# Optimization experiments

Measured on AMD Instinct MI355X. Metric: run time of the kernel, lower is better.

## Reference

```python
import jax, jax.numpy as jnp
import numpy as np

D_MODEL = 256   # dim // 2
DIM = 512
D_INNER = 512   # expand=2 * d_model
D_STATE = 16
D_CONV = 4
DT_RANK = 16    # ceil(d_model/16)
N_LAYERS = 2
H_RES, W_RES = 16, 16
EPS = 1e-5


def silu(v):
    return v * jax.nn.sigmoid(v)


def setup_inputs() -> dict:
    key = jax.random.key(0)
    ks = jax.random.split(key, 12)
    Bsz, T, N = 2, 4, 256
    x = jax.random.normal(ks[0], (Bsz, 1 + T * N, DIM), jnp.float32)
    skip = jax.random.normal(ks[1], (Bsz, 1 + 4 * T * N, D_MODEL), jnp.float32)
    sc = lambda k, shape, s: jax.random.normal(k, shape, jnp.float32) * s
    exp_w = sc(ks[2], (2 * DIM, DIM), 0.02)            # PatchExpanding2D.expansion (no bias)
    ln_g = jnp.ones((DIM // 2,), jnp.float32)
    ln_b = jnp.zeros((DIM // 2,), jnp.float32)
    cls_w = sc(ks[3], (DIM // 2, DIM), 0.02)
    cls_b = jnp.zeros((DIM // 2,), jnp.float32)
    in_proj_w = sc(ks[4], (N_LAYERS, 2 * D_INNER, D_MODEL), 0.02)
    conv_w = sc(ks[5], (N_LAYERS, D_INNER, D_CONV), 0.1)  # depthwise causal conv
    conv_b = jnp.zeros((N_LAYERS, D_INNER), jnp.float32)
    xproj_w = sc(ks[6], (N_LAYERS, DT_RANK + 2 * D_STATE, D_INNER), 0.02)
    dt_w = sc(ks[7], (N_LAYERS, D_INNER, DT_RANK), 0.1)
    dt_b = sc(ks[8], (N_LAYERS, D_INNER), 0.1)
    A_log = jnp.log(jnp.broadcast_to(jnp.arange(1, D_STATE + 1, dtype=jnp.float32), (N_LAYERS, D_INNER, D_STATE)))
    Dp = jnp.ones((N_LAYERS, D_INNER), jnp.float32)
    out_w = sc(ks[9], (N_LAYERS, D_MODEL, D_INNER), 0.02)
    bn_g = jnp.ones((D_MODEL,), jnp.float32)
    bn_b = jnp.zeros((D_MODEL,), jnp.float32)
    return {"x": x, "skip_connection": skip, "exp_w": exp_w, "ln_g": ln_g, "ln_b": ln_b,
            "cls_w": cls_w, "cls_b": cls_b, "in_proj_w": in_proj_w, "conv_w": conv_w,
            "conv_b": conv_b, "xproj_w": xproj_w, "dt_w": dt_w, "dt_b": dt_b,
            "A_log": A_log, "Dp": Dp, "out_w": out_w, "bn_g": bn_g, "bn_b": bn_b,
            "B": 2, "T": 4, "N": 256}


def mamba_layer(u, Wi, cw, cb, Wx, Wdt, bdt, A_log, Dd, Wo):
    # u: [B, L, d_model]
    Bb, L, _ = u.shape
    xz = jnp.einsum('bld,ed->ble', u, Wi)            # [B, L, 2*d_inner]
    xi, z = jnp.split(xz, 2, axis=-1)
    # depthwise causal conv1d (pad left d_conv-1)
    xp = jnp.pad(xi, ((0, 0), (D_CONV - 1, 0), (0, 0)))
    xc = cb + sum(cw[:, k] * xp[:, k:k + L, :] for k in range(D_CONV))
    xi = silu(xc)
    dbc = jnp.einsum('bld,ed->ble', xi, Wx)          # [B, L, dt_rank + 2*d_state]
    dt = dbc[..., :DT_RANK]
    Bm = dbc[..., DT_RANK:DT_RANK + D_STATE]
    Cm = dbc[..., DT_RANK + D_STATE:]
    delta = jax.nn.softplus(jnp.einsum('blr,dr->bld', dt, Wdt) + bdt)  # [B, L, d_inner]
    A = -jnp.exp(A_log)                              # [d_inner, d_state]

    def step(h, inp):
        d_t, B_t, C_t, x_t = inp                     # [B,d], [B,n], [B,n], [B,d]
        h = h * jnp.exp(d_t[..., None] * A) + d_t[..., None] * B_t[:, None, :] * x_t[..., None]
        y = jnp.einsum('bdn,bn->bd', h, C_t)
        return h, y

    h0 = jnp.zeros((Bb, D_INNER, D_STATE), u.dtype)
    xs = (jnp.swapaxes(delta, 0, 1), jnp.swapaxes(Bm, 0, 1),
          jnp.swapaxes(Cm, 0, 1), jnp.swapaxes(xi, 0, 1))
    _, ys = jax.lax.scan(step, h0, xs)               # ys: [L, B, d_inner]
    y = jnp.swapaxes(ys, 0, 1) + xi * Dd
    y = y * silu(z)
    return jnp.einsum('bld,od->blo', y, Wo)          # [B, L, d_model]


def reference(x, skip_connection, exp_w, ln_g, ln_b, cls_w, cls_b, in_proj_w, conv_w,
              conv_b, xproj_w, dt_w, dt_b, A_log, Dp, out_w, bn_g, bn_b, B, T, N):
    cls = x[:B, :1, :]                               # [B, 1, dim]
    toks = x[:, 1:, :].reshape(x.shape[0], T, N, DIM)
    # patch expanding: Linear dim -> 2*dim, then 2x2 pixel shuffle, LayerNorm(dim//2)
    e = jnp.einsum('btnm,em->btne', toks, exp_w)     # [B, T, N, 2*dim]
    m = (2 * DIM) // 4                               # dim // 2
    e = e.reshape(-1, T, H_RES, W_RES, 2, 2, m)
    e = jnp.transpose(e, (0, 1, 2, 4, 3, 5, 6)).reshape(-1, T, 4 * N, m)
    mu = e.mean(-1, keepdims=True)
    var = e.var(-1, keepdims=True)
    e = (e - mu) / jnp.sqrt(var + EPS) * ln_g + ln_b
    e = e.reshape(e.shape[0], T * 4 * N, m)
    cls = jnp.einsum('bom,em->boe', cls, cls_w) + cls_b
    xx = jnp.concatenate([cls, e], axis=1) + skip_connection
    for i in range(N_LAYERS):
        xx = mamba_layer(xx, in_proj_w[i], conv_w[i], conv_b[i], xproj_w[i],
                         dt_w[i], dt_b[i], A_log[i], Dp[i], out_w[i])
    # BatchNorm1d over channels (training-mode batch stats, biased variance)
    mu = xx.mean(axis=(0, 1))
    var = xx.var(axis=(0, 1))
    xx = (xx - mu) / jnp.sqrt(var + EPS) * bn_g + bn_b
    return xx, 4 * N
```

## Files before the change

### kernel.cpp

```cpp
#include <hip/hip_runtime.h>
#include <hip/hip_bf16.h>
#include <math.h>

#define L_TOT 4097
#define BSZ 2
#define ROWS (BSZ*L_TOT)
#define NSEG 128
#define SEGLEN 33

typedef __bf16 bf16x8 __attribute__((ext_vector_type(8)));
typedef float  f32x4  __attribute__((ext_vector_type(4)));
#define ASTR 56
#define AST2 72

__device__ __forceinline__ float sigmoidf_(float v){ return 1.0f/(1.0f+__expf(-v)); }
__device__ __forceinline__ float siluf_(float v){ return v * sigmoidf_(v); }
__device__ __forceinline__ unsigned short bfbits(float f){
    __bf16 h = (__bf16)f;
    return __builtin_bit_cast(unsigned short, h);
}

__global__ __launch_bounds__(256) void cvt4(
    const float* __restrict__ w0, const float* __restrict__ w1,
    const float* __restrict__ w2, const float* __restrict__ w3,
    __bf16* __restrict__ o0, __bf16* __restrict__ o1,
    __bf16* __restrict__ o2, __bf16* __restrict__ o3)
{
    long i = ((long)blockIdx.x*256 + threadIdx.x)*8;
    const float* src; __bf16* dst; long off;
    if (i < 524288)        { src = w0; dst = o0; off = i; }
    else if (i < 1048576)  { src = w1; dst = o1; off = i - 524288; }
    else if (i < 1310720)  { src = w2; dst = o2; off = i - 1048576; }
    else if (i < 1359872)  { src = w3; dst = o3; off = i - 1310720; }
    else return;
    float4 a = *(const float4*)(src+off), b = *(const float4*)(src+off+4);
    bf16x8 o;
    o[0]=(__bf16)a.x; o[1]=(__bf16)a.y; o[2]=(__bf16)a.z; o[3]=(__bf16)a.w;
    o[4]=(__bf16)b.x; o[5]=(__bf16)b.y; o[6]=(__bf16)b.z; o[7]=(__bf16)b.w;
    *(bf16x8*)(dst+off) = o;
}

__global__ __launch_bounds__(256) void cvt_gather_x(
    const float* __restrict__ x, __bf16* __restrict__ out)
{
    long i = ((long)blockIdx.x*256 + threadIdx.x)*8;
    if (i >= 2048L*512) return;
    int row = (int)(i >> 9), col = (int)(i & 511);
    long srow = row + (row >> 10) + 1;
    const float* src = x + srow*512 + col;
    float4 a = *(const float4*)src, b = *(const float4*)(src+4);
    bf16x8 o;
    o[0]=(__bf16)a.x; o[1]=(__bf16)a.y; o[2]=(__bf16)a.z; o[3]=(__bf16)a.w;
    o[4]=(__bf16)b.x; o[5]=(__bf16)b.y; o[6]=(__bf16)b.z; o[7]=(__bf16)b.w;
    *(bf16x8*)(out+i) = o;
}

template<int SMODE>
__global__ __launch_bounds__(256) void gemm_bf16(
    const __bf16* __restrict__ A, const __bf16* __restrict__ W,
    float* __restrict__ C, __bf16* __restrict__ C2, int M, int N, int K)
{
    __shared__ __bf16 Als[128*ASTR];
    __shared__ __bf16 Wls[64*ASTR];
    const int tid = threadIdx.x;
    const int lane = tid & 63, w = tid >> 6;
    const int n0 = blockIdx.x*64, m0 = blockIdx.y*128;

    f32x4 acc[2][4] = {};
    const int arow = tid >> 1, ahalf = tid & 1;
    const int wrow = tid >> 2, wseg = tid & 3;
    const int fr = lane & 15, fc = lane >> 4;

    for (int k0 = 0; k0 < K; k0 += 32) {
        bf16x8 av0 = {}, av1 = {};
        if (m0 + arow < M) {
            const __bf16* src = A + (long)(m0+arow)*K + k0 + ahalf*16;
            av0 = *(const bf16x8*)src;
            av1 = *(const bf16x8*)(src+8);
        }
        bf16x8 wv = *(const bf16x8*)(W + (long)(n0+wrow)*K + k0 + wseg*8);
        __syncthreads();
        *(bf16x8*)&Als[arow*ASTR + ahalf*16]     = av0;
        *(bf16x8*)&Als[arow*ASTR + ahalf*16 + 8] = av1;
        *(bf16x8*)&Wls[wrow*ASTR + wseg*8]       = wv;
        __syncthreads();

        bf16x8 a0 = *(const bf16x8*)&Als[(w*32 +      fr)*ASTR + fc*8];
        bf16x8 a1 = *(const bf16x8*)&Als[(w*32 + 16 + fr)*ASTR + fc*8];
        #pragma unroll
        for (int j = 0; j < 4; j++) {
            bf16x8 bv = *(const bf16x8*)&Wls[(j*16 + fr)*ASTR + fc*8];
            acc[0][j] = __builtin_amdgcn_mfma_f32_16x16x32_bf16(a0, bv, acc[0][j], 0,0,0);
            acc[1][j] = __builtin_amdgcn_mfma_f32_16x16x32_bf16(a1, bv, acc[1][j], 0,0,0);
        }
    }
    #pragma unroll
    for (int i = 0; i < 2; i++) {
        #pragma unroll
        for (int rr = 0; rr < 4; rr++) {
            int grow = m0 + w*32 + i*16 + fc*4 + rr;
            if (grow < M) {
                #pragma unroll
                for (int j = 0; j < 4; j++) {
                    float v = acc[i][j][rr];
                    long o = (long)grow*N + n0 + j*16 + fr;
                    if (SMODE != 2) C[o] = v;
                    if (SMODE != 0) C2[o] = (__bf16)v;
                }
            }
        }
    }
}

__global__ __launch_bounds__(256) void gemm_bf16_128(
    const __bf16* __restrict__ A, const __bf16* __restrict__ W,
    __bf16* __restrict__ C2, int M, int N, int K)
{
    __shared__ __bf16 Als[128*AST2];
    __shared__ __bf16 Wls[128*AST2];
    const int tid = threadIdx.x;
    const int lane = tid & 63, w = tid >> 6;
    const int n0 = blockIdx.x*128, m0 = blockIdx.y*128;
    const int fr = lane & 15, fc = lane >> 4;
    const int row2 = tid >> 1, half = tid & 1;

    f32x4 acc[2][8] = {};

    for (int k0 = 0; k0 < K; k0 += 64) {
        bf16x8 av[4], wv[4];
        const bool aok = (m0 + row2) < M;
        const __bf16* asrc = A + (long)(m0+row2)*K + k0 + half*32;
        const __bf16* wsrc = W + (long)(n0+row2)*K + k0 + half*32;
        #pragma unroll
        for (int e = 0; e < 4; e++) {
            av[e] = aok ? *(const bf16x8*)(asrc + e*8) : (bf16x8){};
            wv[e] = *(const bf16x8*)(wsrc + e*8);
        }
        __syncthreads();
        #pragma unroll
        for (int e = 0; e < 4; e++) {
            *(bf16x8*)&Als[row2*AST2 + half*32 + e*8] = av[e];
            *(bf16x8*)&Wls[row2*AST2 + half*32 + e*8] = wv[e];
        }
        __syncthreads();
        #pragma unroll
        for (int s = 0; s < 2; s++) {
            bf16x8 a0 = *(const bf16x8*)&Als[(w*32 +      fr)*AST2 + s*32 + fc*8];
            bf16x8 a1 = *(const bf16x8*)&Als[(w*32 + 16 + fr)*AST2 + s*32 + fc*8];
            #pragma unroll
            for (int j = 0; j < 8; j++) {
                bf16x8 bv = *(const bf16x8*)&Wls[(j*16 + fr)*AST2 + s*32 + fc*8];
                acc[0][j] = __builtin_amdgcn_mfma_f32_16x16x32_bf16(a0, bv, acc[0][j], 0,0,0);
                acc[1][j] = __builtin_amdgcn_mfma_f32_16x16x32_bf16(a1, bv, acc[1][j], 0,0,0);
            }
        }
    }
    #pragma unroll
    for (int i = 0; i < 2; i++) {
        #pragma unroll
        for (int rr = 0; rr < 4; rr++) {
            int grow = m0 + w*32 + i*16 + fc*4 + rr;
            if (grow < M) {
                #pragma unroll
                for (int j = 0; j < 8; j++)
                    C2[(long)grow*N + n0 + j*16 + fr] = (__bf16)acc[i][j][rr];
            }
        }
    }
}

__global__ __launch_bounds__(128) void gemm_dbc(
    const __bf16* __restrict__ A, const __bf16* __restrict__ W,
    float* __restrict__ C, int M)
{
    __shared__ __bf16 Als[64*ASTR];
    __shared__ __bf16 Wls[48*ASTR];
    const int tid = threadIdx.x;
    const int lane = tid & 63, w = tid >> 6;
    const int m0 = blockIdx.x*64;
    f32x4 acc[2][3] = {};

    const int arow = tid >> 1, ahalf = tid & 1;
    const int fr = lane & 15, fc = lane >> 4;

    for (int k0 = 0; k0 < 512; k0 += 32) {
        bf16x8 av0 = {}, av1 = {};
        if (m0 + arow < M) {
            const __bf16* src = A + (long)(m0+arow)*512 + k0 + ahalf*16;
            av0 = *(const bf16x8*)src;
            av1 = *(const bf16x8*)(src+8);
        }
        bf16x8 wv0 = {}, wv1 = {};
        if (tid < 96) {
            const __bf16* src = W + (long)(tid>>1)*512 + k0 + (tid&1)*16;
            wv0 = *(const bf16x8*)src;
            wv1 = *(const bf16x8*)(src+8);
        }
        __syncthreads();
        *(bf16x8*)&Als[arow*ASTR + ahalf*16]     = av0;
        *(bf16x8*)&Als[arow*ASTR + ahalf*16 + 8] = av1;
        if (tid < 96) {
            *(bf16x8*)&Wls[(tid>>1)*ASTR + (tid&1)*16]     = wv0;
            *(bf16x8*)&Wls[(tid>>1)*ASTR + (tid&1)*16 + 8] = wv1;
        }
        __syncthreads();

        bf16x8 a0 = *(const bf16x8*)&Als[(w*32 +      fr)*ASTR + fc*8];
        bf16x8 a1 = *(const bf16x8*)&Als[(w*32 + 16 + fr)*ASTR + fc*8];
        #pragma unroll
        for (int j = 0; j < 3; j++) {
            bf16x8 bv = *(const bf16x8*)&Wls[(j*16 + fr)*ASTR + fc*8];
            acc[0][j] = __builtin_amdgcn_mfma_f32_16x16x32_bf16(a0, bv, acc[0][j], 0,0,0);
            acc[1][j] = __builtin_amdgcn_mfma_f32_16x16x32_bf16(a1, bv, acc[1][j], 0,0,0);
        }
    }
    #pragma unroll
    for (int i = 0; i < 2; i++) {
        #pragma unroll
        for (int rr = 0; rr < 4; rr++) {
            int grow = m0 + w*32 + i*16 + fc*4 + rr;
            if (grow < M) {
                #pragma unroll
                for (int j = 0; j < 3; j++)
                    C[(long)grow*48 + j*16 + fr] = acc[i][j][rr];
            }
        }
    }
}

__global__ __launch_bounds__(256) void delta_k(
    const float* __restrict__ dbc, const float* __restrict__ Wdt,
    const float* __restrict__ bdt, const __bf16* __restrict__ xib,
    unsigned* __restrict__ pdx)
{
    const int d0 = threadIdx.x, d1 = threadIdx.x + 256;
    const int r0 = blockIdx.x*8;
    f32x4 wa[4], wb[4];
    #pragma unroll
    for (int q = 0; q < 4; q++) {
        wa[q] = *(const f32x4*)(Wdt + d0*16 + q*4);
        wb[q] = *(const f32x4*)(Wdt + d1*16 + q*4);
    }
    const float b0 = bdt[d0], b1 = bdt[d1];
    #pragma unroll
    for (int rr = 0; rr < 8; rr++) {
        int row = r0 + rr;
        if (row >= ROWS) return;
        const f32x4* p = (const f32x4*)(dbc + (long)row*48);
        f32x4 t0 = p[0], t1 = p[1], t2 = p[2], t3 = p[3];
        float s0 = b0, s1 = b1;
        #pragma unroll
        for (int e = 0; e < 4; e++) {
            s0 += wa[0][e]*t0[e] + wa[1][e]*t1[e] + wa[2][e]*t2[e] + wa[3][e]*t3[e];
            s1 += wb[0][e]*t0[e] + wb[1][e]*t1[e] + wb[2][e]*t2[e] + wb[3][e]*t3[e];
        }
        float dl0 = (s0 > 20.f) ? s0 : log1pf(__expf(s0));
        float dl1 = (s1 > 20.f) ? s1 : log1pf(__expf(s1));
        unsigned x0 = __builtin_bit_cast(unsigned short, xib[(long)row*512 + d0]);
        unsigned x1 = __builtin_bit_cast(unsigned short, xib[(long)row*512 + d1]);
        pdx[(long)row*512 + d0] = (unsigned)bfbits(dl0) | (x0 << 16);
        pdx[(long)row*512 + d1] = (unsigned)bfbits(dl1) | (x1 << 16);
    }
}

__global__ __launch_bounds__(256) void rearrange_ln_cls(
    const __bf16* __restrict__ e_buf, const float* __restrict__ x,
    const float* __restrict__ cls_w, const float* __restrict__ cls_b,
    const float* __restrict__ ln_g, const float* __restrict__ ln_b,
    const float* __restrict__ skip, float* __restrict__ xx,
    __bf16* __restrict__ xxb)
{
    const int blk = blockIdx.x;
    const int b = blk / L_TOT;
    const int q = blk % L_TOT;
    const int c = threadIdx.x;

    if (q == 0) {
        __shared__ float xr[512];
        const float* xrow = x + (long)b*1025*512;
        xr[c] = xrow[c]; xr[c+256] = xrow[c+256];
        __syncthreads();
        float acc = cls_b[c];
        const float4* wrow = (const float4*)(cls_w + (long)c*512);
        #pragma unroll 8
        for (int m4 = 0; m4 < 128; m4++) {
            float4 wv = wrow[m4];
            float4 xv = *(const float4*)&xr[m4*4];
            acc += wv.x*xv.x + wv.y*xv.y + wv.z*xv.z + wv.w*xv.w;
        }
        long o = (long)b*L_TOT*256 + c;
        float v = acc + skip[o];
        xx[o] = v; xxb[o] = (__bf16)v;
        return;
    }
    const int t  = (q-1) >> 10;
    const int p  = (q-1) & 1023;
    const int h  = p >> 6;
    const int a  = (p >> 5) & 1;
    const int w  = (p >> 1) & 15;
    const int bb = p & 1;
    const long tok = (long)b*1024 + t*256 + h*16 + w;
    float v = (float)e_buf[tok*1024 + a*512 + bb*256 + c];

    float s = v, s2 = v*v;
    #pragma unroll
    for (int o = 32; o > 0; o >>= 1) { s += __shfl_xor(s, o); s2 += __shfl_xor(s2, o); }
    __shared__ float ps[4], ps2[4];
    __shared__ float mu_s, rs_s;
    const int wv = threadIdx.x >> 6;
    if ((threadIdx.x & 63) == 0) { ps[wv] = s; ps2[wv] = s2; }
    __syncthreads();
    if (threadIdx.x == 0) {
        float S = ps[0]+ps[1]+ps[2]+ps[3];
        float S2 = ps2[0]+ps2[1]+ps2[2]+ps2[3];
        float mu = S * (1.f/256.f);
        float var = S2 * (1.f/256.f) - mu*mu;
        mu_s = mu; rs_s = rsqrtf(var + 1e-5f);
    }
    __syncthreads();
    long o = ((long)b*L_TOT + q)*256 + c;
    float outv = (v - mu_s)*rs_s*ln_g[c] + ln_b[c] + skip[o];
    xx[o] = outv; xxb[o] = (__bf16)outv;
}

__global__ __launch_bounds__(256) void conv_silu_split(
    const __bf16* __restrict__ xzb, const float* __restrict__ cw,
    const float* __restrict__ cb, __bf16* __restrict__ xib,
    __bf16* __restrict__ zsb)
{
    const int tid = threadIdx.x;
    const int c = tid & 127;
    const long r0 = ((long)blockIdx.x*2 + (tid >> 7))*8;
    if (r0 >= ROWS) return;

    if (c < 64) {
        const int d0 = c*8;
        float wreg[4][8], breg[8];
        #pragma unroll
        for (int e = 0; e < 8; e++) {
            breg[e] = cb[d0+e];
            #pragma unroll
            for (int k = 0; k < 4; k++) wreg[k][e] = cw[(d0+e)*4 + k];
        }
        bf16x8 win[4];
        #pragma unroll
        for (int j = 0; j < 3; j++) {
            long rr = r0 - 3 + j;
            win[j] = (rr >= 0) ? *(const bf16x8*)&xzb[rr*1024 + d0] : (bf16x8){};
        }
        #pragma unroll
        for (int rr = 0; rr < 8; rr++) {
            long rl = r0 + rr;
            if (rl >= ROWS) break;
            win[3] = *(const bf16x8*)&xzb[rl*1024 + d0];
            int l = (int)(rl % L_TOT);
            float acc[8];
            #pragma unroll
            for (int e = 0; e < 8; e++) acc[e] = breg[e];
            #pragma unroll
            for (int k = 0; k < 4; k++) {
                if (l + k - 3 >= 0) {
                    #pragma unroll
                    for (int e = 0; e < 8; e++)
                        acc[e] += wreg[k][e]*(float)win[k][e];
                }
            }
            bf16x8 o;
            #pragma unroll
            for (int e = 0; e < 8; e++) o[e] = (__bf16)siluf_(acc[e]);
            *(bf16x8*)&xib[rl*512 + d0] = o;
            win[0] = win[1]; win[1] = win[2]; win[2] = win[3];
        }
    } else {
        const int d0 = (c - 64)*8;
        #pragma unroll
        for (int rr = 0; rr < 8; rr++) {
            long rl = r0 + rr;
            if (rl >= ROWS) break;
            bf16x8 v = *(const bf16x8*)&xzb[rl*1024 + 512 + d0];
            bf16x8 o;
            #pragma unroll
            for (int e = 0; e < 8; e++) o[e] = (__bf16)siluf_((float)v[e]);
            *(bf16x8*)&zsb[rl*512 + d0] = o;
        }
    }
}

__global__ __launch_bounds__(256) void scan_p1(
    const unsigned* __restrict__ pdx,
    const float* __restrict__ dbc, const float* __restrict__ A_log,
    float* __restrict__ segH, float* __restrict__ segP)
{
    __shared__ unsigned pdxS[SEGLEN*64];
    __shared__ float bS[SEGLEN*16];
    const int blk = blockIdx.x;
    const int seg = blk >> 4;
    const int b   = (blk >> 3) & 1;
    const int dbase = (blk & 7)*64;
    const int tid = threadIdx.x;
    const int l0 = seg*SEGLEN;
    const int nl = min(l0 + SEGLEN, L_TOT) - l0;
    const int nlc = nl > 0 ? nl : 0;

    for (int cc = tid; cc < nlc*16; cc += 256) {
        int l = cc >> 4, qq = cc & 15;
        *(uint4*)&pdxS[l*64 + qq*4] =
            *(const uint4*)&pdx[((long)b*L_TOT + l0 + l)*512 + dbase + qq*4];
    }
    for (int cc = tid; cc < nlc*4; cc += 256) {
        int l = cc >> 2, qq = cc & 3;
        *(f32x4*)&bS[l*16 + qq*4] =
            *(const f32x4*)&dbc[((long)b*L_TOT + l0 + l)*48 + 16 + qq*4];
    }
    __syncthreads();

    const int dl_ = tid >> 2;
    const int d = dbase + dl_;
    const int ng = tid & 3;
    f32x4 Al = *(const f32x4*)(A_log + d*16 + ng*4);
    float Ar[4] = {-__expf(Al[0]), -__expf(Al[1]), -__expf(Al[2]), -__expf(Al[3])};
    float h[4] = {0,0,0,0};
    float P[4] = {1,1,1,1};
    for (int l = 0; l < nlc; l++) {
        unsigned v = pdxS[l*64 + dl_];
        float dl = __uint_as_float(v << 16);
        float xv = __uint_as_float(v & 0xffff0000u);
        f32x4 Bv = *(const f32x4*)&bS[l*16 + ng*4];
        float dx = dl*xv;
        #pragma unroll
        for (int n = 0; n < 4; n++) {
            float E = __expf(dl*Ar[n]);
            h[n] = h[n]*E + dx*Bv[n];
            P[n] *= E;
        }
    }
    long off = ((long)(seg*2 + b)*512 + d)*16 + ng*4;
    *(f32x4*)&segH[off] = f32x4{h[0],h[1],h[2],h[3]};
    *(f32x4*)&segP[off] = f32x4{P[0],P[1],P[2],P[3]};
}

__global__ __launch_bounds__(256) void scan_p2(
    float* __restrict__ segH, const float* __restrict__ segP)
{
    const int idx = blockIdx.x*256 + threadIdx.x;
    float carry = 0.f;
    for (int s0 = 0; s0 < NSEG; s0 += 8) {
        float hh[8], pp[8];
        #pragma unroll
        for (int j = 0; j < 8; j++) {
            long o = (long)(s0+j)*16384 + idx;
            hh[j] = segH[o]; pp[j] = segP[o];
        }
        #pragma unroll
        for (int j = 0; j < 8; j++) {
            long o = (long)(s0+j)*16384 + idx;
            segH[o] = carry;
            carry = pp[j]*carry + hh[j];
        }
    }
}

__global__ __launch_bounds__(256) void scan_p3(
    const unsigned* __restrict__ pdx,
    const float* __restrict__ dbc, const float* __restrict__ A_log,
    const float* __restrict__ segH, const float* __restrict__ Dp,
    const __bf16* __restrict__ zsb, __bf16* __restrict__ yb)
{
    __shared__ unsigned pdxS[SEGLEN*64];
    __shared__ float bcS[SEGLEN*32];
    __shared__ __bf16 zS[SEGLEN*64];
    __shared__ __bf16 yS[SEGLEN*64];
    const int blk = blockIdx.x;
    const int seg = blk >> 4;
    const int b   = (blk >> 3) & 1;
    const int dbase = (blk & 7)*64;
    const int tid = threadIdx.x;
    const int l0 = seg*SEGLEN;
    const int nl = min(l0 + SEGLEN, L_TOT) - l0;
    const int nlc = nl > 0 ? nl : 0;
    if (nlc == 0) return;

    for (int cc = tid; cc < nlc*16; cc += 256) {
        int l = cc >> 4, qq = cc & 15;
        *(uint4*)&pdxS[l*64 + qq*4] =
            *(const uint4*)&pdx[((long)b*L_TOT + l0 + l)*512 + dbase + qq*4];
    }
    for (int cc = tid; cc < nlc*8; cc += 256) {
        int l = cc >> 3, qq = cc & 7;
        *(f32x4*)&bcS[l*32 + qq*4] =
            *(const f32x4*)&dbc[((long)b*L_TOT + l0 + l)*48 + 16 + qq*4];
    }
    for (int cc = tid; cc < nlc*8; cc += 256) {
        int l = cc >> 3, qq = cc & 7;
        *(bf16x8*)&zS[l*64 + qq*8] =
            *(const bf16x8*)&zsb[((long)b*L_TOT + l0 + l)*512 + dbase + qq*8];
    }
    __syncthreads();

    const int dl_ = tid >> 2;
    const int d = dbase + dl_;
    const int ng = tid & 3;
    f32x4 Al = *(const f32x4*)(A_log + d*16 + ng*4);
    float Ar[4] = {-__expf(Al[0]), -__expf(Al[1]), -__expf(Al[2]), -__expf(Al[3])};
    long off = ((long)(seg*2 + b)*512 + d)*16 + ng*4;
    f32x4 h4 = *(const f32x4*)&segH[off];
    float h[4] = {h4[0], h4[1], h4[2], h4[3]};
    const float Dd = Dp[d];
    for (int l = 0; l < nlc; l++) {
        unsigned v = pdxS[l*64 + dl_];
        float dl = __uint_as_float(v << 16);
        float xv = __uint_as_float(v & 0xffff0000u);
        f32x4 Bv = *(const f32x4*)&bcS[l*32 + ng*4];
        f32x4 Cv = *(const f32x4*)&bcS[l*32 + 16 + ng*4];
        float dx = dl*xv;
        float y = 0.f;
        #pragma unroll
        for (int n = 0; n < 4; n++) {
            float E = __expf(dl*Ar[n]);
            h[n] = h[n]*E + dx*Bv[n];
            y += h[n]*Cv[n];
        }
        y += __shfl_xor(y, 1);
        y += __shfl_xor(y, 2);
        if (ng == 0) {
            float z = (float)zS[l*64 + dl_];
            yS[l*64 + dl_] = (__bf16)((y + xv*Dd)*z);
        }
    }
    __syncthreads();
    for (int cc = tid; cc < nlc*8; cc += 256) {
        int l = cc >> 3, qq = cc & 7;
        *(bf16x8*)&yb[((long)b*L_TOT + l0 + l)*512 + dbase + qq*8] =
            *(bf16x8*)&yS[l*64 + qq*8];
    }
}

__global__ void zero_stats(float* __restrict__ stats) { stats[threadIdx.x] = 0.f; }

__global__ __launch_bounds__(256) void bn_reduce(
    const float* __restrict__ xx, float* __restrict__ stats)
{
    const int c = threadIdx.x;
    float s = 0.f, s2 = 0.f;
    for (int r = blockIdx.x; r < ROWS; r += gridDim.x) {
        float v = xx[(long)r*256 + c];
        s += v; s2 += v*v;
    }
    atomicAdd(&stats[c], s);
    atomicAdd(&stats[256 + c], s2);
}

__global__ __launch_bounds__(256) void bn_apply(
    const float* __restrict__ xx, const float* __restrict__ stats,
    const float* __restrict__ g, const float* __restrict__ bta,
    float* __restrict__ out)
{
    long idx = (long)blockIdx.x*256 + threadIdx.x;
    if (idx == 0) out[(long)ROWS*256] = 1024.0f;
    if (idx >= (long)ROWS*256) return;
    int c = (int)(idx & 255);
    float mu = stats[c] * (1.f/ROWS);
    float var = stats[256 + c] * (1.f/ROWS) - mu*mu;
    out[idx] = (xx[idx] - mu)*rsqrtf(var + 1e-5f)*g[c] + bta[c];
}

extern "C" void kernel_launch(void* const* d_in, const int* in_sizes, int n_in,
                              void* d_out, int out_size, void* d_ws, size_t ws_size,
                              hipStream_t stream)
{
    const float* x        = (const float*)d_in[0];
    const float* skip     = (const float*)d_in[1];
    const float* exp_w    = (const float*)d_in[2];
    const float* ln_g     = (const float*)d_in[3];
    const float* ln_b     = (const float*)d_in[4];
    const float* cls_w    = (const float*)d_in[5];
    const float* cls_b    = (const float*)d_in[6];
    const float* in_proj_w= (const float*)d_in[7];
    const float* conv_w   = (const float*)d_in[8];
    const float* conv_b   = (const float*)d_in[9];
    const float* xproj_w  = (const float*)d_in[10];
    const float* dt_w     = (const float*)d_in[11];
    const float* dt_b     = (const float*)d_in[12];
    const float* A_log    = (const float*)d_in[13];
    const float* Dp       = (const float*)d_in[14];
    const float* out_w    = (const float*)d_in[15];
    const float* bn_g     = (const float*)d_in[16];
    const float* bn_b     = (const float*)d_in[17];

    float* ws = (float*)d_ws;
    float* xx    = ws;
    float* dbc   = xx + 2097664;
    float* segH  = dbc + 393312;
    float* segP  = segH + 2097152;
    float* stats = segP + 2097152;
    unsigned* pdx = (unsigned*)(stats + 512);
    __bf16* expWb = (__bf16*)(pdx + 4195328);
    __bf16* inWb  = expWb + 524288;
    __bf16* outWb = inWb + 524288;
    __bf16* xpWb  = outWb + 262144;
    __bf16* xxb   = xpWb + 49152;
    __bf16* xzb   = xxb + 2097664;
    __bf16* e_b   = xzb;
    __bf16* xib   = xzb + 8390656;
    __bf16* Axb   = xib;
    __bf16* zsb   = xib + 4195328;
    __bf16* yb    = zsb + 4195328;
    float* out    = (float*)d_out;

    cvt4<<<(1359872/8 + 255)/256, 256, 0, stream>>>(
        exp_w, in_proj_w, out_w, xproj_w, expWb, inWb, outWb, xpWb);
    cvt_gather_x<<<(1048576/8)/256, 256, 0, stream>>>(x, Axb);

    gemm_bf16<2><<<dim3(16, 16), 256, 0, stream>>>(
        Axb, expWb, nullptr, e_b, 2048, 1024, 512);
    rearrange_ln_cls<<<ROWS, 256, 0, stream>>>(
        e_b, x, cls_w, cls_b, ln_g, ln_b, skip, xx, xxb);

    for (int layer = 0; layer < 2; layer++) {
        gemm_bf16_128<<<dim3(8, 65), 256, 0, stream>>>(
            xxb, inWb + layer*262144, xzb, ROWS, 1024, 256);
        conv_silu_split<<<513, 256, 0, stream>>>(
            xzb, conv_w + layer*512*4, conv_b + layer*512, xib, zsb);
        gemm_dbc<<<(ROWS + 63)/64, 128, 0, stream>>>(
            xib, xpWb + layer*24576, dbc, ROWS);
        delta_k<<<(ROWS + 7)/8, 256, 0, stream>>>(
            dbc, dt_w + layer*512*16, dt_b + layer*512, xib, pdx);
        scan_p1<<<NSEG*16, 256, 0, stream>>>(
            pdx, dbc, A_log + layer*512*16, segH, segP);
        scan_p2<<<64, 256, 0, stream>>>(segH, segP);
        scan_p3<<<NSEG*16, 256, 0, stream>>>(
            pdx, dbc, A_log + layer*512*16, segH, Dp + layer*512, zsb, yb);
        if (layer == 0) {
            gemm_bf16<1><<<dim3(4, 65), 256, 0, stream>>>(
                yb, outWb, xx, xxb, ROWS, 256, 512);
        } else {
            gemm_bf16<0><<<dim3(4, 65), 256, 0, stream>>>(
                yb, outWb + 131072, xx, nullptr, ROWS, 256, 512);
        }
    }

    zero_stats<<<1, 512, 0, stream>>>(stats);
    bn_reduce<<<128, 256, 0, stream>>>(xx, stats);
    bn_apply<<<((long)ROWS*256 + 255)/256 + 1, 256, 0, stream>>>(xx, stats, bn_g, bn_b, out);
}
```

Before: 406.9 us.

## Fuse silu into in_proj epilogue, merge xproj with delta, drop fp32 residual

The in_proj GEMM now writes the x half and silu(z) half into separate bf16 buffers, so the conv kernel only handles the x half. The x-projection GEMM and the delta/softplus computation are fused into one kernel that stages a full 64-row tile in shared memory and emits B/C plus the packed delta/x words. The fp32 residual copy xx is dropped in favour of bf16 only, and LayerNorm/cls uses one wavefront per row with vector loads. These changes cut launches and global traffic, at the cost of lower precision in the final BatchNorm input and a large shared-memory footprint in the fused xproj kernel.

Result: slower. 498.8 us (+22.6%).

```diff
diff --git a/kernel.cpp b/kernel.cpp
--- a/kernel.cpp
+++ b/kernel.cpp
@@ -12,6 +12,7 @@
 typedef float  f32x4  __attribute__((ext_vector_type(4)));
 #define ASTR 56
 #define AST2 72
+#define XSTR 520
 
 __device__ __forceinline__ float sigmoidf_(float v){ return 1.0f/(1.0f+__expf(-v)); }
 __device__ __forceinline__ float siluf_(float v){ return v * sigmoidf_(v); }
@@ -55,10 +56,9 @@
     *(bf16x8*)(out+i) = o;
 }
 
-template<int SMODE>
 __global__ __launch_bounds__(256) void gemm_bf16(
     const __bf16* __restrict__ A, const __bf16* __restrict__ W,
-    float* __restrict__ C, __bf16* __restrict__ C2, int M, int N, int K)
+    __bf16* __restrict__ C2, int M, int N, int K)
 {
     __shared__ __bf16 Als[128*ASTR];
     __shared__ __bf16 Wls[64*ASTR];
@@ -101,20 +101,16 @@
             int grow = m0 + w*32 + i*16 + fc*4 + rr;
             if (grow < M) {
                 #pragma unroll
-                for (int j = 0; j < 4; j++) {
-                    float v = acc[i][j][rr];
-                    long o = (long)grow*N + n0 + j*16 + fr;
-                    if (SMODE != 2) C[o] = v;
-                    if (SMODE != 0) C2[o] = (__bf16)v;
-                }
+                for (int j = 0; j < 4; j++)
+                    C2[(long)grow*N + n0 + j*16 + fr] = (__bf16)acc[i][j][rr];
             }
         }
     }
 }
 
-__global__ __launch_bounds__(256) void gemm_bf16_128(
+__global__ __launch_bounds__(256) void gemm_inproj(
     const __bf16* __restrict__ A, const __bf16* __restrict__ W,
-    __bf16* __restrict__ C2, int M, int N, int K)
+    __bf16* __restrict__ xhb, __bf16* __restrict__ zsb, int M, int K)
 {
     __shared__ __bf16 Als[128*AST2];
     __shared__ __bf16 Wls[128*AST2];
@@ -155,111 +151,94 @@
             }
         }
     }
+    const bool xhalf = (n0 < 512);
+    const int cbase = xhalf ? n0 : (n0 - 512);
     #pragma unroll
     for (int i = 0; i < 2; i++) {
         #pragma unroll
         for (int rr = 0; rr < 4; rr++) {
             int grow = m0 + w*32 + i*16 + fc*4 + rr;
             if (grow < M) {
-                #pragma unroll
-                for (int j = 0; j < 8; j++)
-                    C2[(long)grow*N + n0 + j*16 + fr] = (__bf16)acc[i][j][rr];
+                if (xhalf) {
+                    #pragma unroll
+                    for (int j = 0; j < 8; j++)
+                        xhb[(long)grow*512 + cbase + j*16 + fr] = (__bf16)acc[i][j][rr];
+                } else {
+                    #pragma unroll
+                    for (int j = 0; j < 8; j++)
+                        zsb[(long)grow*512 + cbase + j*16 + fr] = (__bf16)siluf_(acc[i][j][rr]);
+                }
             }
         }
     }
 }
 
-__global__ __launch_bounds__(128) void gemm_dbc(
-    const __bf16* __restrict__ A, const __bf16* __restrict__ W,
-    float* __restrict__ C, int M)
-{
-    __shared__ __bf16 Als[64*ASTR];
-    __shared__ __bf16 Wls[48*ASTR];
+__global__ __launch_bounds__(256) void xproj_fused(
+    const __bf16* __restrict__ xib, const __bf16* __restrict__ Wx,
+    const float* __restrict__ Wdt, const float* __restrict__ bdt,
+    float* __restrict__ BC, unsigned* __restrict__ pdx)
+{
+    __shared__ __bf16 At[64*XSTR];
+    __shared__ __bf16 Wls[48*XSTR];
+    __shared__ float dtS[64*16];
     const int tid = threadIdx.x;
     const int lane = tid & 63, w = tid >> 6;
-    const int m0 = blockIdx.x*64;
-    f32x4 acc[2][3] = {};
-
-    const int arow = tid >> 1, ahalf = tid & 1;
+    const long r0 = (long)blockIdx.x*64;
     const int fr = lane & 15, fc = lane >> 4;
 
+    for (int idx = tid; idx < 64*64; idx += 256) {
+        int r = idx >> 6, c8 = idx & 63;
+        bf16x8 v = (r0 + r < ROWS) ? *(const bf16x8*)&xib[(r0+r)*512 + c8*8]
+                                   : (bf16x8){};
+        *(bf16x8*)&At[r*XSTR + c8*8] = v;
+    }
+    for (int idx = tid; idx < 48*64; idx += 256) {
+        int r = idx >> 6, c8 = idx & 63;
+        *(bf16x8*)&Wls[r*XSTR + c8*8] = *(const bf16x8*)&Wx[r*512 + c8*8];
+    }
+    __syncthreads();
+
+    f32x4 acc[3] = {};
     for (int k0 = 0; k0 < 512; k0 += 32) {
-        bf16x8 av0 = {}, av1 = {};
-        if (m0 + arow < M) {
-            const __bf16* src = A + (long)(m0+arow)*512 + k0 + ahalf*16;
-            av0 = *(const bf16x8*)src;
-            av1 = *(const bf16x8*)(src+8);
-        }
-        bf16x8 wv0 = {}, wv1 = {};
-        if (tid < 96) {
-            const __bf16* src = W + (long)(tid>>1)*512 + k0 + (tid&1)*16;
-            wv0 = *(const bf16x8*)src;
-            wv1 = *(const bf16x8*)(src+8);
-        }
-        __syncthreads();
-        *(bf16x8*)&Als[arow*ASTR + ahalf*16]     = av0;
-        *(bf16x8*)&Als[arow*ASTR + ahalf*16 + 8] = av1;
-        if (tid < 96) {
-            *(bf16x8*)&Wls[(tid>>1)*ASTR + (tid&1)*16]     = wv0;
-            *(bf16x8*)&Wls[(tid>>1)*ASTR + (tid&1)*16 + 8] = wv1;
-        }
-        __syncthreads();
-
-        bf16x8 a0 = *(const bf16x8*)&Als[(w*32 +      fr)*ASTR + fc*8];
-        bf16x8 a1 = *(const bf16x8*)&Als[(w*32 + 16 + fr)*ASTR + fc*8];
+        bf16x8 a = *(const bf16x8*)&At[(w*16 + fr)*XSTR + k0 + fc*8];
         #pragma unroll
         for (int j = 0; j < 3; j++) {
-            bf16x8 bv = *(const bf16x8*)&Wls[(j*16 + fr)*ASTR + fc*8];
-            acc[0][j] = __builtin_amdgcn_mfma_f32_16x16x32_bf16(a0, bv, acc[0][j], 0,0,0);
-            acc[1][j] = __builtin_amdgcn_mfma_f32_16x16x32_bf16(a1, bv, acc[1][j], 0,0,0);
-        }
-    }
-    #pragma unroll
-    for (int i = 0; i < 2; i++) {
-        #pragma unroll
-        for (int rr = 0; rr < 4; rr++) {
-            int grow = m0 + w*32 + i*16 + fc*4 + rr;
-            if (grow < M) {
-                #pragma unroll
-                for (int j = 0; j < 3; j++)
-                    C[(long)grow*48 + j*16 + fr] = acc[i][j][rr];
-            }
-        }
-    }
-}
-
-__global__ __launch_bounds__(256) void delta_k(
-    const float* __restrict__ dbc, const float* __restrict__ Wdt,
-    const float* __restrict__ bdt, const __bf16* __restrict__ xib,
-    unsigned* __restrict__ pdx)
-{
-    const int d0 = threadIdx.x, d1 = threadIdx.x + 256;
-    const int r0 = blockIdx.x*8;
-    f32x4 wa[4], wb[4];
-    #pragma unroll
-    for (int q = 0; q < 4; q++) {
-        wa[q] = *(const f32x4*)(Wdt + d0*16 + q*4);
-        wb[q] = *(const f32x4*)(Wdt + d1*16 + q*4);
-    }
-    const float b0 = bdt[d0], b1 = bdt[d1];
-    #pragma unroll
-    for (int rr = 0; rr < 8; rr++) {
-        int row = r0 + rr;
-        if (row >= ROWS) return;
-        const f32x4* p = (const f32x4*)(dbc + (long)row*48);
-        f32x4 t0 = p[0], t1 = p[1], t2 = p[2], t3 = p[3];
-        float s0 = b0, s1 = b1;
-        #pragma unroll
-        for (int e = 0; e < 4; e++) {
-            s0 += wa[0][e]*t0[e] + wa[1][e]*t1[e] + wa[2][e]*t2[e] + wa[3][e]*t3[e];
-            s1 += wb[0][e]*t0[e] + wb[1][e]*t1[e] + wb[2][e]*t2[e] + wb[3][e]*t3[e];
-        }
-        float dl0 = (s0 > 20.f) ? s0 : log1pf(__expf(s0));
-        float dl1 = (s1 > 20.f) ? s1 : log1pf(__expf(s1));
-        unsigned x0 = __builtin_bit_cast(unsigned short, xib[(long)row*512 + d0]);
-        unsigned x1 = __builtin_bit_cast(unsigned short, xib[(long)row*512 + d1]);
-        pdx[(long)row*512 + d0] = (unsigned)bfbits(dl0) | (x0 << 16);
-        pdx[(long)row*512 + d1] = (unsigned)bfbits(dl1) | (x1 << 16);
+            bf16x8 bv = *(const bf16x8*)&Wls[(j*16 + fr)*XSTR + k0 + fc*8];
+            acc[j] = __builtin_amdgcn_mfma_f32_16x16x32_bf16(a, bv, acc[j], 0,0,0);
+        }
+    }
+    #pragma unroll
+    for (int rr = 0; rr < 4; rr++) {
+        int lrow = w*16 + fc*4 + rr;
+        long grow = r0 + lrow;
+        dtS[lrow*16 + fr] = acc[0][rr];
+        if (grow < ROWS) {
+            BC[grow*32 + fr]      = acc[1][rr];
+            BC[grow*32 + 16 + fr] = acc[2][rr];
+        }
+    }
+    __syncthreads();
+
+    #pragma unroll
+    for (int rep = 0; rep < 2; rep++) {
+        const int d = tid + rep*256;
+        f32x4 wa0 = *(const f32x4*)(Wdt + d*16);
+        f32x4 wa1 = *(const f32x4*)(Wdt + d*16 + 4);
+        f32x4 wa2 = *(const f32x4*)(Wdt + d*16 + 8);
+        f32x4 wa3 = *(const f32x4*)(Wdt + d*16 + 12);
+        const float bia = bdt[d];
+        for (int r = 0; r < 64; r++) {
+            long grow = r0 + r;
+            if (grow >= ROWS) break;
+            const float* dt = &dtS[r*16];
+            float s = bia;
+            #pragma unroll
+            for (int e = 0; e < 4; e++)
+                s += wa0[e]*dt[e] + wa1[e]*dt[4+e] + wa2[e]*dt[8+e] + wa3[e]*dt[12+e];
+            float dl = (s > 20.f) ? s : log1pf(__expf(s));
+            unsigned xb = __builtin_bit_cast(unsigned short, At[r*XSTR + d]);
+            pdx[grow*512 + d] = (unsigned)bfbits(dl) | (xb << 16);
+        }
     }
 }
 
@@ -267,128 +246,119 @@
     const __bf16* __restrict__ e_buf, const float* __restrict__ x,
     const float* __restrict__ cls_w, const float* __restrict__ cls_b,
     const float* __restrict__ ln_g, const float* __restrict__ ln_b,
-    const float* __restrict__ skip, float* __restrict__ xx,
-    __bf16* __restrict__ xxb)
-{
-    const int blk = blockIdx.x;
-    const int b = blk / L_TOT;
-    const int q = blk % L_TOT;
-    const int c = threadIdx.x;
+    const float* __restrict__ skip, __bf16* __restrict__ xxb)
+{
+    const int wv = threadIdx.x >> 6, lane = threadIdx.x & 63;
+    const int qg = blockIdx.x*4 + wv;
+    if (qg >= ROWS) return;
+    const int b = qg / L_TOT, q = qg % L_TOT;
+    const long obase = (long)qg*256;
 
     if (q == 0) {
-        __shared__ float xr[512];
-        const float* xrow = x + (long)b*1025*512;
-        xr[c] = xrow[c]; xr[c+256] = xrow[c+256];
-        __syncthreads();
-        float acc = cls_b[c];
-        const float4* wrow = (const float4*)(cls_w + (long)c*512);
-        #pragma unroll 8
-        for (int m4 = 0; m4 < 128; m4++) {
-            float4 wv = wrow[m4];
-            float4 xv = *(const float4*)&xr[m4*4];
-            acc += wv.x*xv.x + wv.y*xv.y + wv.z*xv.z + wv.w*xv.w;
-        }
-        long o = (long)b*L_TOT*256 + c;
-        float v = acc + skip[o];
-        xx[o] = v; xxb[o] = (__bf16)v;
+        const float* xr = x + (long)b*1025*512;
+        #pragma unroll
+        for (int i = 0; i < 4; i++) {
+            int c = lane + i*64;
+            float acc = cls_b[c];
+            const float4* wr = (const float4*)(cls_w + (long)c*512);
+            #pragma unroll 8
+            for (int m4 = 0; m4 < 128; m4++) {
+                float4 wv4 = wr[m4];
+                float4 xv4 = *(const float4*)&xr[m4*4];
+                acc += wv4.x*xv4.x + wv4.y*xv4.y + wv4.z*xv4.z + wv4.w*xv4.w;
+            }
+            xxb[obase + c] = (__bf16)(acc + skip[obase + c]);
+        }
         return;
     }
     const int t  = (q-1) >> 10;
     const int p  = (q-1) & 1023;
     const int h  = p >> 6;
     const int a  = (p >> 5) & 1;
-    const int w  = (p >> 1) & 15;
+    const int w_ = (p >> 1) & 15;
     const int bb = p & 1;
-    const long tok = (long)b*1024 + t*256 + h*16 + w;
-    float v = (float)e_buf[tok*1024 + a*512 + bb*256 + c];
-
-    float s = v, s2 = v*v;
+    const long tok = (long)b*1024 + t*256 + h*16 + w_;
+    const __bf16* src = e_buf + tok*1024 + a*512 + bb*256 + lane*4;
+    float v[4];
+    {
+        ushort2 u0 = *(const ushort2*)src;
+        ushort2 u1 = *(const ushort2*)(src+2);
+        v[0] = (float)__builtin_bit_cast(__bf16, u0.x);
+        v[1] = (float)__builtin_bit_cast(__bf16, u0.y);
+        v[2] = (float)__builtin_bit_cast(__bf16, u1.x);
+        v[3] = (float)__builtin_bit_cast(__bf16, u1.y);
+    }
+    float s = v[0]+v[1]+v[2]+v[3];
+    float s2 = v[0]*v[0]+v[1]*v[1]+v[2]*v[2]+v[3]*v[3];
     #pragma unroll
     for (int o = 32; o > 0; o >>= 1) { s += __shfl_xor(s, o); s2 += __shfl_xor(s2, o); }
-    __shared__ float ps[4], ps2[4];
-    __shared__ float mu_s, rs_s;
-    const int wv = threadIdx.x >> 6;
-    if ((threadIdx.x & 63) == 0) { ps[wv] = s; ps2[wv] = s2; }
-    __syncthreads();
-    if (threadIdx.x == 0) {
-        float S = ps[0]+ps[1]+ps[2]+ps[3];
-        float S2 = ps2[0]+ps2[1]+ps2[2]+ps2[3];
-        float mu = S * (1.f/256.f);
-        float var = S2 * (1.f/256.f) - mu*mu;
-        mu_s = mu; rs_s = rsqrtf(var + 1e-5f);
-    }
-    __syncthreads();
-    long o = ((long)b*L_TOT + q)*256 + c;
-    float outv = (v - mu_s)*rs_s*ln_g[c] + ln_b[c] + skip[o];
-    xx[o] = outv; xxb[o] = (__bf16)outv;
-}
-
-__global__ __launch_bounds__(256) void conv_silu_split(
-    const __bf16* __restrict__ xzb, const float* __restrict__ cw,
-    const float* __restrict__ cb, __bf16* __restrict__ xib,
-    __bf16* __restrict__ zsb)
+    float mu = s * (1.f/256.f);
+    float rs = rsqrtf(s2*(1.f/256.f) - mu*mu + 1e-5f);
+    const int c0 = lane*4;
+    float4 sk = *(const float4*)&skip[obase + c0];
+    float skv[4] = {sk.x, sk.y, sk.z, sk.w};
+    __bf16 ov[4];
+    #pragma unroll
+    for (int i = 0; i < 4; i++)
+        ov[i] = (__bf16)((v[i] - mu)*rs*ln_g[c0+i] + ln_b[c0+i] + skv[i]);
+    *(ushort2*)&xxb[obase + c0]     = make_ushort2(
+        __builtin_bit_cast(unsigned short, ov[0]),
+        __builtin_bit_cast(unsigned short, ov[1]));
+    *(ushort2*)&xxb[obase + c0 + 2] = make_ushort2(
+        __builtin_bit_cast(unsigned short, ov[2]),
+        __builtin_bit_cast(unsigned short, ov[3]));
+}
+
+__global__ __launch_bounds__(256) void conv_silu(
+    const __bf16* __restrict__ xhb, const float* __restrict__ cw,
+    const float* __restrict__ cb, __bf16* __restrict__ xib)
 {
     const int tid = threadIdx.x;
-    const int c = tid & 127;
-    const long r0 = ((long)blockIdx.x*2 + (tid >> 7))*8;
+    const int c = tid & 63;
+    const long r0 = ((long)blockIdx.x*4 + (tid >> 6))*8;
     if (r0 >= ROWS) return;
-
-    if (c < 64) {
-        const int d0 = c*8;
-        float wreg[4][8], breg[8];
-        #pragma unroll
-        for (int e = 0; e < 8; e++) {
-            breg[e] = cb[d0+e];
-            #pragma unroll
-            for (int k = 0; k < 4; k++) wreg[k][e] = cw[(d0+e)*4 + k];
-        }
-        bf16x8 win[4];
-        #pragma unroll
-        for (int j = 0; j < 3; j++) {
-            long rr = r0 - 3 + j;
-            win[j] = (rr >= 0) ? *(const bf16x8*)&xzb[rr*1024 + d0] : (bf16x8){};
-        }
-        #pragma unroll
-        for (int rr = 0; rr < 8; rr++) {
-            long rl = r0 + rr;
-            if (rl >= ROWS) break;
-            win[3] = *(const bf16x8*)&xzb[rl*1024 + d0];
-            int l = (int)(rl % L_TOT);
-            float acc[8];
-            #pragma unroll
-            for (int e = 0; e < 8; e++) acc[e] = breg[e];
-            #pragma unroll
-            for (int k = 0; k < 4; k++) {
-                if (l + k - 3 >= 0) {
-                    #pragma unroll
-                    for (int e = 0; e < 8; e++)
-                        acc[e] += wreg[k][e]*(float)win[k][e];
-                }
+    const int d0 = c*8;
+    float wreg[4][8], breg[8];
+    #pragma unroll
+    for (int e = 0; e < 8; e++) {
+        breg[e] = cb[d0+e];
+        #pragma unroll
+        for (int k = 0; k < 4; k++) wreg[k][e] = cw[(d0+e)*4 + k];
+    }
+    bf16x8 win[4];
+    #pragma unroll
+    for (int j = 0; j < 3; j++) {
+        long rr = r0 - 3 + j;
+        win[j] = (rr >= 0) ? *(const bf16x8*)&xhb[rr*512 + d0] : (bf16x8){};
+    }
+    #pragma unroll
+    for (int rr = 0; rr < 8; rr++) {
+        long rl = r0 + rr;
+        if (rl >= ROWS) break;
+        win[3] = *(const bf16x8*)&xhb[rl*512 + d0];
+        int l = (int)(rl % L_TOT);
+        float acc[8];
+        #pragma unroll
+        for (int e = 0; e < 8; e++) acc[e] = breg[e];
+        #pragma unroll
+        for (int k = 0; k < 4; k++) {
+            if (l + k - 3 >= 0) {
+                #pragma unroll
+                for (int e = 0; e < 8; e++)
+                    acc[e] += wreg[k][e]*(float)win[k][e];
             }
-            bf16x8 o;
-            #pragma unroll
-            for (int e = 0; e < 8; e++) o[e] = (__bf16)siluf_(acc[e]);
-            *(bf16x8*)&xib[rl*512 + d0] = o;
-            win[0] = win[1]; win[1] = win[2]; win[2] = win[3];
-        }
-    } else {
-        const int d0 = (c - 64)*8;
-        #pragma unroll
-        for (int rr = 0; rr < 8; rr++) {
-            long rl = r0 + rr;
-            if (rl >= ROWS) break;
-            bf16x8 v = *(const bf16x8*)&xzb[rl*1024 + 512 + d0];
-            bf16x8 o;
-            #pragma unroll
-            for (int e = 0; e < 8; e++) o[e] = (__bf16)siluf_((float)v[e]);
-            *(bf16x8*)&zsb[rl*512 + d0] = o;
-        }
+        }
+        bf16x8 o;
+        #pragma unroll
+        for (int e = 0; e < 8; e++) o[e] = (__bf16)siluf_(acc[e]);
+        *(bf16x8*)&xib[rl*512 + d0] = o;
+        win[0] = win[1]; win[1] = win[2]; win[2] = win[3];
     }
 }
 
 __global__ __launch_bounds__(256) void scan_p1(
     const unsigned* __restrict__ pdx,
-    const float* __restrict__ dbc, const float* __restrict__ A_log,
+    const float* __restrict__ BC, const float* __restrict__ A_log,
     float* __restrict__ segH, float* __restrict__ segP)
 {
     __shared__ unsigned pdxS[SEGLEN*64];
@@ -410,7 +380,7 @@
     for (int cc = tid; cc < nlc*4; cc += 256) {
         int l = cc >> 2, qq = cc & 3;
         *(f32x4*)&bS[l*16 + qq*4] =
-            *(const f32x4*)&dbc[((long)b*L_TOT + l0 + l)*48 + 16 + qq*4];
+            *(const f32x4*)&BC[((long)b*L_TOT + l0 + l)*32 + qq*4];
     }
     __syncthreads();
 
@@ -462,7 +432,7 @@
 
 __global__ __launch_bounds__(256) void scan_p3(
     const unsigned* __restrict__ pdx,
-    const float* __restrict__ dbc, const float* __restrict__ A_log,
+    const float* __restrict__ BC, const float* __restrict__ A_log,
     const float* __restrict__ segH, const float* __restrict__ Dp,
     const __bf16* __restrict__ zsb, __bf16* __restrict__ yb)
 {
@@ -488,7 +458,7 @@
     for (int cc = tid; cc < nlc*8; cc += 256) {
         int l = cc >> 3, qq = cc & 7;
         *(f32x4*)&bcS[l*32 + qq*4] =
-            *(const f32x4*)&dbc[((long)b*L_TOT + l0 + l)*48 + 16 + qq*4];
+            *(const f32x4*)&BC[((long)b*L_TOT + l0 + l)*32 + qq*4];
     }
     for (int cc = tid; cc < nlc*8; cc += 256) {
         int l = cc >> 3, qq = cc & 7;
@@ -538,12 +508,12 @@
 __global__ void zero_stats(float* __restrict__ stats) { stats[threadIdx.x] = 0.f; }
 
 __global__ __launch_bounds__(256) void bn_reduce(
-    const float* __restrict__ xx, float* __restrict__ stats)
+    const __bf16* __restrict__ xxb, float* __restrict__ stats)
 {
     const int c = threadIdx.x;
     float s = 0.f, s2 = 0.f;
     for (int r = blockIdx.x; r < ROWS; r += gridDim.x) {
-        float v = xx[(long)r*256 + c];
+        float v = (float)xxb[(long)r*256 + c];
         s += v; s2 += v*v;
     }
     atomicAdd(&stats[c], s);
@@ -551,7 +521,7 @@
 }
 
 __global__ __launch_bounds__(256) void bn_apply(
-    const float* __restrict__ xx, const float* __restrict__ stats,
+    const __bf16* __restrict__ xxb, const float* __restrict__ stats,
     const float* __restrict__ g, const float* __restrict__ bta,
     float* __restrict__ out)
 {
@@ -561,7 +531,7 @@
     int c = (int)(idx & 255);
     float mu = stats[c] * (1.f/ROWS);
     float var = stats[256 + c] * (1.f/ROWS) - mu*mu;
-    out[idx] = (xx[idx] - mu)*rsqrtf(var + 1e-5f)*g[c] + bta[c];
+    out[idx] = ((float)xxb[idx] - mu)*rsqrtf(var + 1e-5f)*g[c] + bta[c];
 }
 
 extern "C" void kernel_launch(void* const* d_in, const int* in_sizes, int n_in,
@@ -588,9 +558,8 @@
     const float* bn_b     = (const float*)d_in[17];
 
     float* ws = (float*)d_ws;
-    float* xx    = ws;
-    float* dbc   = xx + 2097664;
-    float* segH  = dbc + 393312;
+    float* BC    = ws;
+    float* segH  = BC + 262208;
     float* segP  = segH + 2097152;
     float* stats = segP + 2097152;
     unsigned* pdx = (unsigned*)(stats + 512);
@@ -599,47 +568,42 @@
     __bf16* outWb = inWb + 524288;
     __bf16* xpWb  = outWb + 262144;
     __bf16* xxb   = xpWb + 49152;
-    __bf16* xzb   = xxb + 2097664;
-    __bf16* e_b   = xzb;
-    __bf16* xib   = xzb + 8390656;
+    __bf16* xhb   = xxb + 2097664;
+    __bf16* e_b   = xhb;
+    __bf16* zsb   = xhb + 4195328;
+    __bf16* xib   = zsb + 4195328;
     __bf16* Axb   = xib;
-    __bf16* zsb   = xib + 4195328;
-    __bf16* yb    = zsb + 4195328;
+    __bf16* yb    = xib + 4195328;
     float* out    = (float*)d_out;
 
     cvt4<<<(1359872/8 + 255)/256, 256, 0, stream>>>(
         exp_w, in_proj_w, out_w, xproj_w, expWb, inWb, outWb, xpWb);
     cvt_gather_x<<<(1048576/8)/256, 256, 0, stream>>>(x, Axb);
 
-    gemm_bf16<2><<<dim3(16, 16), 256, 0, stream>>>(
-        Axb, expWb, nullptr, e_b, 2048, 1024, 512);
-    rearrange_ln_cls<<<ROWS, 256, 0, stream>>>(
-        e_b, x, cls_w, cls_b, ln_g, ln_b, skip, xx, xxb);
+    gemm_bf16<<<dim3(16, 16), 256, 0, stream>>>(
+        Axb, expWb, e_b, 2048, 1024, 512);
+    rearrange_ln_cls<<<(ROWS + 3)/4, 256, 0, stream>>>(
+        e_b, x, cls_w, cls_b, ln_g, ln_b, skip, xxb);
 
     for (int layer = 0; layer < 2; layer++) {
-        gemm_bf16_128<<<dim3(8, 65), 256, 0, stream>>>(
-            xxb, inWb + layer*262144, xzb, ROWS, 1024, 256);
-        conv_silu_split<<<513, 256, 0, stream>>>(
-            xzb, conv_w + layer*512*4, conv_b + layer*512, xib, zsb);
-        gemm_dbc<<<(ROWS + 63)/64, 128, 0, stream>>>(
-            xib, xpWb + layer*24576, dbc, ROWS);
-        delta_k<<<(ROWS + 7)/8, 256, 0, stream>>>(
-            dbc, dt_w + layer*512*16, dt_b + layer*512, xib, pdx);
+        gemm_inproj<<<dim3(8, 65), 256, 0, stream>>>(
+            xxb, inWb + layer*262144, xhb, zsb, ROWS, 256);
+        conv_silu<<<(ROWS + 31)/32, 256, 0, stream>>>(
+            xhb, conv_w + layer*512*4, conv_b + layer*512, xib);
+        xproj_fused<<<(ROWS + 63)/64, 256, 0, stream>>>(
+            xib, xpWb + layer*24576, dt_w + layer*512*16, dt_b + layer*512,
+            BC, pdx);
         scan_p1<<<NSEG*16, 256, 0, stream>>>(
-            pdx, dbc, A_log + layer*512*16, segH, segP);
+            pdx, BC, A_log + layer*512*16, segH, segP);
         scan_p2<<<64, 256, 0, stream>>>(segH, segP);
         scan_p3<<<NSEG*16, 256, 0, stream>>>(
-            pdx, dbc, A_log + layer*512*16, segH, Dp + layer*512, zsb, yb);
-        if (layer == 0) {
-            gemm_bf16<1><<<dim3(4, 65), 256, 0, stream>>>(
-                yb, outWb, xx, xxb, ROWS, 256, 512);
-        } else {
-            gemm_bf16<0><<<dim3(4, 65), 256, 0, stream>>>(
-                yb, outWb + 131072, xx, nullptr, ROWS, 256, 512);
-        }
+            pdx, BC, A_log + layer*512*16, segH, Dp + layer*512, zsb, yb);
+        gemm_bf16<<<dim3(4, 65), 256, 0, stream>>>(
+            yb, outWb + layer*131072, xxb, ROWS, 256, 512);
     }
 
     zero_stats<<<1, 512, 0, stream>>>(stats);
-    bn_reduce<<<128, 256, 0, stream>>>(xx, stats);
-    bn_apply<<<((long)ROWS*256 + 255)/256 + 1, 256, 0, stream>>>(xx, stats, bn_g, bn_b, out);
-}
+    bn_reduce<<<128, 256, 0, stream>>>(xxb, stats);
+    bn_apply<<<((long)ROWS*256 + 255)/256 + 1, 256, 0, stream>>>(
+        xxb, stats, bn_g, bn_b, out);
+}
```
